# Optimization experiments

Hardware: AMD Instinct MI355X
Metric: run time of the kernel (lower is better)

Reference implementation:

```python
import jax, jax.numpy as jnp
import numpy as np

EMBEDDING_SIZE = 50
MAX_DOCUMENT_LENGTH = 100
MAX_LABEL = 15
VOCAB = 200000
HID = 1024
BATCH = 4096


def setup_inputs() -> dict:
    key = jax.random.key(0)
    ks = jax.random.split(key, 8)
    x = jax.random.randint(ks[0], (BATCH, MAX_DOCUMENT_LENGTH), 0, VOCAB)
    emb_table = jax.random.normal(ks[1], (VOCAB, EMBEDDING_SIZE), jnp.float32) * 0.05
    # Keras GRUCell (reset_after=True): kernel [E,3H], recurrent_kernel [H,3H],
    # bias [2,3H] split into input bias and recurrent bias; gate order z, r, h.
    kernel = jax.random.normal(ks[2], (EMBEDDING_SIZE, 3 * HID), jnp.float32) * (1.0 / np.sqrt(EMBEDDING_SIZE))
    rec_kernel = jax.random.normal(ks[3], (HID, 3 * HID), jnp.float32) * (1.0 / np.sqrt(HID))
    bias_i = jnp.zeros((3 * HID,), jnp.float32)
    bias_r = jnp.zeros((3 * HID,), jnp.float32)
    Wd = jax.random.normal(ks[4], (HID, MAX_LABEL), jnp.float32) * (1.0 / np.sqrt(HID))
    bd = jnp.zeros((MAX_LABEL,), jnp.float32)
    return {"x": x, "drop_rate": 0, "emb_table": emb_table, "kernel": kernel,
            "rec_kernel": rec_kernel, "bias_i": bias_i, "bias_r": bias_r,
            "Wd": Wd, "bd": bd}


def _gru_scan(emb, kernel, rec_kernel, bias_i, bias_r):
    # emb: [B,T,E] -> time-major [T,B,E]
    emb_t = jnp.transpose(emb, (1, 0, 2))
    B = emb.shape[0]
    h0 = jnp.zeros((B, HID), emb.dtype)

    def step(h, x_t):
        xp = x_t @ kernel + bias_i            # [B,3H]
        hp = h @ rec_kernel + bias_r          # [B,3H]
        xz, xr, xh = jnp.split(xp, 3, axis=-1)
        hz, hr, hh = jnp.split(hp, 3, axis=-1)
        z = jax.nn.sigmoid(xz + hz)
        r = jax.nn.sigmoid(xr + hr)
        hcand = jnp.tanh(xh + r * hh)
        h_new = z * h + (1.0 - z) * hcand
        return h_new, None

    h_last, _ = jax.lax.scan(step, h0, emb_t)
    return h_last


def reference(x, drop_rate, emb_table, kernel, rec_kernel, bias_i, bias_r, Wd, bd):
    emb = emb_table[x]                         # [B,T,E]
    encoding = _gru_scan(emb, kernel, rec_kernel, bias_i, bias_r)  # [B,H]
    if drop_rate > 0:                          # drop_rate is a static Python int
        keep = 1.0 - float(drop_rate)
        mask = jax.random.bernoulli(jax.random.key(1), keep, encoding.shape)
        encoding = jnp.where(mask, encoding / keep, 0.0)
    logits = encoding @ Wd + bd                # [B,15]
    return logits
```

## Files before the change

### kernel.cpp

```cpp
#include <hip/hip_runtime.h>
#include <stdint.h>

#define H_DIM   1024
#define G3      3072
#define EMB     50
#define TSTEPS  100
#define NB      4096
#define NLABEL  15

typedef __bf16 bf16x8 __attribute__((ext_vector_type(8)));
typedef float  f32x4  __attribute__((ext_vector_type(4)));
typedef int    i32x4  __attribute__((ext_vector_type(4)));

__device__ inline uint16_t f2bf(float f) {
  uint32_t u = __builtin_bit_cast(uint32_t, f);
  u += 0x7FFFu + ((u >> 16) & 1u);
  return (uint16_t)(u >> 16);
}

__device__ inline void gld16(const void* g, void* l) {
  __builtin_amdgcn_global_load_lds(
      (const __attribute__((address_space(1))) uint32_t*)g,
      (__attribute__((address_space(3))) uint32_t*)l, 16, 0, 0);
}

#define VM(n) do { asm volatile("s_waitcnt vmcnt(" #n ")" ::: "memory"); \
                   __builtin_amdgcn_sched_barrier(0); } while (0)
#define LGKM0() do { asm volatile("s_waitcnt lgkmcnt(0)" ::: "memory"); \
                     __builtin_amdgcn_sched_barrier(0); } while (0)
#define BARF() do { __builtin_amdgcn_s_barrier(); \
                    asm volatile("" ::: "memory"); } while (0)
#define GLDB(dst, addr, OFF) \
  asm volatile("global_load_dwordx4 %0, %1, off offset:" OFF \
               : "=&v"(dst) : "v"(addr) : "memory")


__global__ __launch_bounds__(256) void prep_recT(const float* __restrict__ rec,
                                                 uint16_t* __restrict__ recT) {
  __shared__ uint16_t st[64][72];
  const int n0 = blockIdx.x * 64;
  const int k0 = blockIdx.y * 64;
  const int tid = threadIdx.x;
#pragma unroll
  for (int i = 0; i < 16; ++i) {
    int idx = tid + i * 256;
    int r = idx >> 6;
    int c = idx & 63;
    st[c][r] = f2bf(rec[(size_t)(k0 + r) * G3 + n0 + c]);
  }
  __syncthreads();
#pragma unroll
  for (int i = 0; i < 16; ++i) {
    int idx = tid + i * 256;
    int r = idx >> 6;
    int c = idx & 63;
    recT[(size_t)(n0 + r) * H_DIM + k0 + c] = st[r][c];
  }
}

__global__ __launch_bounds__(256) void prep_kerT(const float* __restrict__ ker,
                                                 uint16_t* __restrict__ kerT) {
  int n = blockIdx.x * 4 + (threadIdx.x >> 6);
  int k = threadIdx.x & 63;
  float v = (k < EMB) ? ker[(size_t)k * G3 + n] : 0.f;
  kerT[(size_t)n * 64 + k] = f2bf(v);
}

__global__ __launch_bounds__(256) void prep_pack(const uint16_t* __restrict__ recT,
                                                 const uint16_t* __restrict__ kerT,
                                                 uint16_t* __restrict__ Bpk) {
  int cid = blockIdx.x * 256 + threadIdx.x;
  int lane = cid & 63;
  int r = cid >> 6;
  int ks = r & 1; r >>= 1;
  int wv = r & 3; r >>= 2;
  int g  = r % 3; r /= 3;
  int kt = r % 17;
  int colblk = r / 17;
  int n  = g * H_DIM + colblk * 64 + wv * 16 + (lane & 15);
  int kk = ks * 32 + (lane >> 4) * 8;
  const uint16_t* src = (kt < 16) ? recT + (size_t)n * H_DIM + kt * 64 + kk
                                  : kerT + (size_t)n * 64 + kk;
  *reinterpret_cast<i32x4*>(Bpk + (size_t)cid * 8) =
      *reinterpret_cast<const i32x4*>(src);
}

__global__ __launch_bounds__(256) void prep_embt(const int* __restrict__ x,
                                                 const float* __restrict__ tab,
                                                 uint16_t* __restrict__ embt) {
  int idx = blockIdx.x * 256 + threadIdx.x;
  int g = idx >> 5;
  int p = idx & 31;
  int t = g >> 12;
  int b = g & 4095;
  int row = x[b * TSTEPS + t];
  float2 v;
  if (p < 25) v = *reinterpret_cast<const float2*>(tab + (size_t)row * EMB + 2 * p);
  else { v.x = 0.f; v.y = 0.f; }
  uint32_t packed = (uint32_t)f2bf(v.x) | ((uint32_t)f2bf(v.y) << 16);
  *reinterpret_cast<uint32_t*>(embt + (size_t)g * 64 + 2 * p) = packed;
}

__global__ __launch_bounds__(256, 2) void gru_step_kernel(
    const uint16_t* __restrict__ hb_prev,
    float* __restrict__ hf,
    uint16_t* __restrict__ hb_next,
    const uint16_t* __restrict__ Bpk,
    const uint16_t* __restrict__ embt,
    const float* __restrict__ bias_i,
    const float* __restrict__ bias_r) {
  __shared__ __align__(16) uint16_t sA2[2][128 * 64];

  const int tid  = threadIdx.x;
  const int lane = tid & 63;
  const int wv   = tid >> 6;
  const int bid  = blockIdx.x;
  const int xk = bid & 7, slot = bid >> 3;
  const int rowblk = (xk >> 1) * 8 + (slot >> 3);
  const int colblk = (xk & 1) * 8 + (slot & 7);
  const int r0 = rowblk * 128;
  const int j0 = colblk * 64;

  const int swz8 = 8 * ((lane & 7) ^ (lane >> 3));

  bf16x8 af[8][2];
  i32x4  bfv[3][2];
  f32x4 accZ[8], accR[8], accH[8], accX[8];
#pragma unroll
  for (int m = 0; m < 8; ++m) {
    accZ[m] = (f32x4){0.f, 0.f, 0.f, 0.f};
    accR[m] = (f32x4){0.f, 0.f, 0.f, 0.f};
    accH[m] = (f32x4){0.f, 0.f, 0.f, 0.f};
    accX[m] = (f32x4){0.f, 0.f, 0.f, 0.f};
  }

  const uint16_t* pB[3];
#pragma unroll
  for (int g = 0; g < 3; ++g)
    pB[g] = Bpk + (size_t)colblk * 17 * 12288 + g * 4096 + wv * 1024 + lane * 8;

  auto stageA = [&](int t) {
    const int abuf = t & 1;
#pragma unroll
    for (int i = 0; i < 4; ++i) {
      int chunk = wv * 4 + i;
      int row = chunk * 8 + (lane >> 3);
      const uint16_t* src = (t < 16)
          ? hb_prev + (size_t)(r0 + row) * H_DIM + t * 64 + swz8
          : embt + (size_t)(r0 + row) * 64 + swz8;
      gld16(src, &sA2[abuf][(chunk * 64 + lane) * 8]);
    }
  };
  auto readA = [&](int t) {
    const int abuf = t & 1;
#pragma unroll
    for (int ks = 0; ks < 2; ++ks) {
      const int colswz = (ks * 32 + (lane >> 4) * 8) ^ ((lane & 7) << 3);
#pragma unroll
      for (int mf = 0; mf < 8; ++mf)
        af[mf][ks] = *reinterpret_cast<const bf16x8*>(
            &sA2[abuf][(mf * 16 + (lane & 15)) * 64 + colswz]);
    }
  };

#define ISSUE_BG(g) do { \
    GLDB(bfv[g][0], pB[g], "0");  GLDB(bfv[g][1], pB[g], "1024"); \
  } while (0)
#define MFG(g, ACC) do { \
    __builtin_amdgcn_s_setprio(1); \
    _Pragma("unroll") for (int ks = 0; ks < 2; ++ks) \
    _Pragma("unroll") for (int mf = 0; mf < 8; ++mf) \
      ACC[mf] = __builtin_amdgcn_mfma_f32_16x16x32_bf16( \
          af[mf][ks], __builtin_bit_cast(bf16x8, bfv[g][ks]), \
          ACC[mf], 0, 0, 0); \
    __builtin_amdgcn_s_setprio(0); \
  } while (0)
#define ADV_B() do { _Pragma("unroll") \
    for (int g = 0; g < 3; ++g) pB[g] += 12288; } while (0)

  stageA(0); stageA(1);
  ISSUE_BG(0); ISSUE_BG(1); ISSUE_BG(2);
  ADV_B();
  VM(6);
  BARF();
  readA(0);

  for (int t = 0; t < 15; ++t) {
    stageA(t + 2);
    VM(8);
    MFG(0, accZ); ISSUE_BG(0);
    VM(8);
    MFG(1, accR); ISSUE_BG(1);
    VM(8);
    MFG(2, accH); ISSUE_BG(2);
    ADV_B();
    readA(t + 1);
    LGKM0();
    VM(6);
    BARF();
  }

  VM(4);  MFG(0, accZ); ISSUE_BG(0);
  VM(4);  MFG(1, accR); ISSUE_BG(1);
  VM(4);  MFG(2, accH); ISSUE_BG(2);
  readA(16);
  LGKM0();
  VM(4);  MFG(0, accZ);
  VM(2);  MFG(1, accR);
  VM(0);  MFG(2, accX);

#undef ISSUE_BG
#undef MFG
#undef ADV_B

  {
    const int col = j0 + wv * 16 + (lane & 15);
    const float b_z = bias_i[col] + bias_r[col];
    const float b_r = bias_i[H_DIM + col] + bias_r[H_DIM + col];
    const float bih = bias_i[2 * H_DIM + col];
    const float brh = bias_r[2 * H_DIM + col];
#pragma unroll
    for (int mf = 0; mf < 8; ++mf) {
#pragma unroll
      for (int q = 0; q < 4; ++q) {
        int row = r0 + mf * 16 + (lane >> 4) * 4 + q;
        float z  = 1.f / (1.f + __expf(-(accZ[mf][q] + b_z)));
        float rr = 1.f / (1.f + __expf(-(accR[mf][q] + b_r)));
        float pre = accX[mf][q] + bih + rr * (accH[mf][q] + brh);
        float hc  = 2.f / (1.f + __expf(-2.f * pre)) - 1.f;
        size_t idx = (size_t)row * H_DIM + col;
        float hold = hf[idx];
        float hnew = z * hold + (1.f - z) * hc;
        hf[idx] = hnew;
        hb_next[idx] = f2bf(hnew);
      }
    }
  }
}

__global__ __launch_bounds__(64) void logits_kernel(const float* __restrict__ hf,
                                                    const float* __restrict__ Wd,
                                                    const float* __restrict__ bd,
                                                    float* __restrict__ out) {
  int b = blockIdx.x;
  int l = threadIdx.x;
  float p[NLABEL];
#pragma unroll
  for (int o = 0; o < NLABEL; ++o) p[o] = 0.f;
  for (int kb = 0; kb < 16; ++kb) {
    int k = kb * 64 + l;
    float hv = hf[(size_t)b * H_DIM + k];
#pragma unroll
    for (int o = 0; o < NLABEL; ++o) p[o] += hv * Wd[k * NLABEL + o];
  }
#pragma unroll
  for (int o = 0; o < NLABEL; ++o) {
#pragma unroll
    for (int s = 32; s; s >>= 1) p[o] += __shfl_xor(p[o], s);
  }
  if (l == 0) {
#pragma unroll
    for (int o = 0; o < NLABEL; ++o) out[(size_t)b * NLABEL + o] = p[o] + bd[o];
  }
}

extern "C" void kernel_launch(void* const* d_in, const int* in_sizes, int n_in,
                              void* d_out, int out_size, void* d_ws, size_t ws_size,
                              hipStream_t stream) {
  const int*   x          = (const int*)d_in[0];
  const float* emb_table  = (const float*)d_in[2];
  const float* kernel_w   = (const float*)d_in[3];
  const float* rec_kernel = (const float*)d_in[4];
  const float* bias_i     = (const float*)d_in[5];
  const float* bias_r     = (const float*)d_in[6];
  const float* Wd         = (const float*)d_in[7];
  const float* bd         = (const float*)d_in[8];
  float* out = (float*)d_out;

  char* ws = (char*)d_ws;
  size_t off = 0;
  auto alloc = [&](size_t bytes) {
    char* p = ws + off;
    off += (bytes + 255) & ~(size_t)255;
    return p;
  };
  float*    hf   = (float*)alloc((size_t)NB * H_DIM * 4);
  uint16_t* hb0  = (uint16_t*)alloc((size_t)NB * H_DIM * 2);
  uint16_t* hb1  = (uint16_t*)alloc((size_t)NB * H_DIM * 2);
  uint16_t* recT = (uint16_t*)alloc((size_t)G3 * H_DIM * 2);
  uint16_t* kerT = (uint16_t*)alloc((size_t)G3 * 64 * 2);
  uint16_t* embt = (uint16_t*)alloc((size_t)TSTEPS * NB * 64 * 2);
  uint16_t* Bpk  = (uint16_t*)alloc((size_t)16 * 17 * 12288 * 2);
  if (off > ws_size) return;

  hipMemsetAsync(hf, 0, (size_t)NB * H_DIM * 4, stream);
  hipMemsetAsync(hb0, 0, (size_t)NB * H_DIM * 2, stream);

  prep_recT<<<dim3(G3 / 64, H_DIM / 64), 256, 0, stream>>>(rec_kernel, recT);
  prep_kerT<<<G3 / 4, 256, 0, stream>>>(kernel_w, kerT);
  prep_pack<<<1632, 256, 0, stream>>>(recT, kerT, Bpk);
  prep_embt<<<TSTEPS * NB * 32 / 256, 256, 0, stream>>>(x, emb_table, embt);

  uint16_t* hb[2] = {hb0, hb1};
  for (int t = 0; t < TSTEPS; ++t) {
    gru_step_kernel<<<512, 256, 0, stream>>>(
        hb[t & 1], hf, hb[(t + 1) & 1], Bpk,
        embt + (size_t)t * NB * 64, bias_i, bias_r);
  }
  logits_kernel<<<NB, 64, 0, stream>>>(hf, Wd, bd, out);
}
```

Measured before the change: 3.296 ms.

## Split GRU step block across eight waves with triple-buffered A tiles

Each GRU step block now runs 512 threads as a 2x4 wave grid instead of 4 waves. Each wave computes 64 rows by 16 columns, so per-wave accumulators and A fragments are halved. The B weight packing is reordered to match the new wave-to-column mapping. The LDS A staging moves to three buffers, with the barrier placed before the LDS read, so the next stage's loads can overlap without a write-after-read hazard. In exchange, B fragments are loaded twice per block (once per row-half wave), and the launch bound of 4 blocks per CU may squeeze registers or exceed the LDS budget.

New measurement: 3.413 ms. 3.6% more time.

```diff
diff --git a/kernel.cpp b/kernel.cpp
--- a/kernel.cpp
+++ b/kernel.cpp
@@ -73,11 +73,12 @@
   int lane = cid & 63;
   int r = cid >> 6;
   int ks = r & 1; r >>= 1;
-  int wv = r & 3; r >>= 2;
+  int nf = r & 1; r >>= 1;
+  int wn = r & 1; r >>= 1;
   int g  = r % 3; r /= 3;
   int kt = r % 17;
   int colblk = r / 17;
-  int n  = g * H_DIM + colblk * 64 + wv * 16 + (lane & 15);
+  int n  = g * H_DIM + colblk * 64 + wn * 32 + nf * 16 + (lane & 15);
   int kk = ks * 32 + (lane >> 4) * 8;
   const uint16_t* src = (kt < 16) ? recT + (size_t)n * H_DIM + kt * 64 + kk
                                   : kerT + (size_t)n * 64 + kk;
@@ -101,7 +102,7 @@
   *reinterpret_cast<uint32_t*>(embt + (size_t)g * 64 + 2 * p) = packed;
 }
 
-__global__ __launch_bounds__(256, 2) void gru_step_kernel(
+__global__ __launch_bounds__(512, 4) void gru_step_kernel(
     const uint16_t* __restrict__ hb_prev,
     float* __restrict__ hf,
     uint16_t* __restrict__ hb_next,
@@ -109,11 +110,13 @@
     const uint16_t* __restrict__ embt,
     const float* __restrict__ bias_i,
     const float* __restrict__ bias_r) {
-  __shared__ __align__(16) uint16_t sA2[2][128 * 64];
+  __shared__ __align__(16) uint16_t sA3[3][128 * 64];
 
   const int tid  = threadIdx.x;
   const int lane = tid & 63;
-  const int wv   = tid >> 6;
+  const int wid  = tid >> 6;
+  const int wm   = wid >> 2;
+  const int wn   = wid & 3;
   const int bid  = blockIdx.x;
   const int xk = bid & 7, slot = bid >> 3;
   const int rowblk = (xk >> 1) * 8 + (slot >> 3);
@@ -123,11 +126,11 @@
 
   const int swz8 = 8 * ((lane & 7) ^ (lane >> 3));
 
-  bf16x8 af[8][2];
-  i32x4  bfv[3][2];
-  f32x4 accZ[8], accR[8], accH[8], accX[8];
-#pragma unroll
-  for (int m = 0; m < 8; ++m) {
+  bf16x8 af[4][2];
+  i32x4  bfr[3][2];
+  f32x4 accZ[4], accR[4], accH[4], accX[4];
+#pragma unroll
+  for (int m = 0; m < 4; ++m) {
     accZ[m] = (f32x4){0.f, 0.f, 0.f, 0.f};
     accR[m] = (f32x4){0.f, 0.f, 0.f, 0.f};
     accH[m] = (f32x4){0.f, 0.f, 0.f, 0.f};
@@ -137,41 +140,41 @@
   const uint16_t* pB[3];
 #pragma unroll
   for (int g = 0; g < 3; ++g)
-    pB[g] = Bpk + (size_t)colblk * 17 * 12288 + g * 4096 + wv * 1024 + lane * 8;
+    pB[g] = Bpk + (size_t)colblk * 17 * 12288 + (g * 8 + wn * 2) * 512 + lane * 8;
 
   auto stageA = [&](int t) {
-    const int abuf = t & 1;
-#pragma unroll
-    for (int i = 0; i < 4; ++i) {
-      int chunk = wv * 4 + i;
+    const int abuf = t % 3;
+#pragma unroll
+    for (int i = 0; i < 2; ++i) {
+      int chunk = wid * 2 + i;
       int row = chunk * 8 + (lane >> 3);
       const uint16_t* src = (t < 16)
           ? hb_prev + (size_t)(r0 + row) * H_DIM + t * 64 + swz8
           : embt + (size_t)(r0 + row) * 64 + swz8;
-      gld16(src, &sA2[abuf][(chunk * 64 + lane) * 8]);
+      gld16(src, &sA3[abuf][(chunk * 64 + lane) * 8]);
     }
   };
   auto readA = [&](int t) {
-    const int abuf = t & 1;
+    const int abuf = t % 3;
 #pragma unroll
     for (int ks = 0; ks < 2; ++ks) {
       const int colswz = (ks * 32 + (lane >> 4) * 8) ^ ((lane & 7) << 3);
 #pragma unroll
-      for (int mf = 0; mf < 8; ++mf)
+      for (int mf = 0; mf < 4; ++mf)
         af[mf][ks] = *reinterpret_cast<const bf16x8*>(
-            &sA2[abuf][(mf * 16 + (lane & 15)) * 64 + colswz]);
+            &sA3[abuf][(wm * 64 + mf * 16 + (lane & 15)) * 64 + colswz]);
     }
   };
 
 #define ISSUE_BG(g) do { \
-    GLDB(bfv[g][0], pB[g], "0");  GLDB(bfv[g][1], pB[g], "1024"); \
+    GLDB(bfr[g][0], pB[g], "0");  GLDB(bfr[g][1], pB[g], "1024"); \
   } while (0)
 #define MFG(g, ACC) do { \
     __builtin_amdgcn_s_setprio(1); \
     _Pragma("unroll") for (int ks = 0; ks < 2; ++ks) \
-    _Pragma("unroll") for (int mf = 0; mf < 8; ++mf) \
+    _Pragma("unroll") for (int mf = 0; mf < 4; ++mf) \
       ACC[mf] = __builtin_amdgcn_mfma_f32_16x16x32_bf16( \
-          af[mf][ks], __builtin_bit_cast(bf16x8, bfv[g][ks]), \
+          af[mf][ks], __builtin_bit_cast(bf16x8, bfr[g][ks]), \
           ACC[mf], 0, 0, 0); \
     __builtin_amdgcn_s_setprio(0); \
   } while (0)
@@ -181,28 +184,32 @@
   stageA(0); stageA(1);
   ISSUE_BG(0); ISSUE_BG(1); ISSUE_BG(2);
   ADV_B();
-  VM(6);
+  VM(8);
   BARF();
   readA(0);
+  LGKM0();
 
   for (int t = 0; t < 15; ++t) {
     stageA(t + 2);
-    VM(8);
+    VM(6);
     MFG(0, accZ); ISSUE_BG(0);
-    VM(8);
+    VM(6);
     MFG(1, accR); ISSUE_BG(1);
-    VM(8);
+    VM(6);
     MFG(2, accH); ISSUE_BG(2);
     ADV_B();
+    BARF();
     readA(t + 1);
     LGKM0();
-    VM(6);
-    BARF();
-  }
-
-  VM(4);  MFG(0, accZ); ISSUE_BG(0);
-  VM(4);  MFG(1, accR); ISSUE_BG(1);
-  VM(4);  MFG(2, accH); ISSUE_BG(2);
+  }
+
+  VM(4);
+  MFG(0, accZ); ISSUE_BG(0);
+  VM(4);
+  MFG(1, accR); ISSUE_BG(1);
+  VM(4);
+  MFG(2, accH); ISSUE_BG(2);
+  BARF();
   readA(16);
   LGKM0();
   VM(4);  MFG(0, accZ);
@@ -214,16 +221,16 @@
 #undef ADV_B
 
   {
-    const int col = j0 + wv * 16 + (lane & 15);
+    const int col = j0 + wn * 16 + (lane & 15);
     const float b_z = bias_i[col] + bias_r[col];
     const float b_r = bias_i[H_DIM + col] + bias_r[H_DIM + col];
     const float bih = bias_i[2 * H_DIM + col];
     const float brh = bias_r[2 * H_DIM + col];
 #pragma unroll
-    for (int mf = 0; mf < 8; ++mf) {
+    for (int mf = 0; mf < 4; ++mf) {
 #pragma unroll
       for (int q = 0; q < 4; ++q) {
-        int row = r0 + mf * 16 + (lane >> 4) * 4 + q;
+        int row = r0 + wm * 64 + mf * 16 + (lane >> 4) * 4 + q;
         float z  = 1.f / (1.f + __expf(-(accZ[mf][q] + b_z)));
         float rr = 1.f / (1.f + __expf(-(accR[mf][q] + b_r)));
         float pre = accX[mf][q] + bih + rr * (accH[mf][q] + brh);
@@ -303,7 +310,7 @@
 
   uint16_t* hb[2] = {hb0, hb1};
   for (int t = 0; t < TSTEPS; ++t) {
-    gru_step_kernel<<<512, 256, 0, stream>>>(
+    gru_step_kernel<<<512, 512, 0, stream>>>(
         hb[t & 1], hf, hb[(t + 1) & 1], Bpk,
         embt + (size_t)t * NB * 64, bias_i, bias_r);
   }
```
